# Optimization experiments

Measured on AMD Instinct MI355X. Metric: run time of the kernel, lower is better.

Reference implementation:

```python
import jax, jax.numpy as jnp
import numpy as np

T, K_FR, K_D, A = 2000, 400, 400, 100
EPS = 1e-24


def setup_inputs() -> dict:
    key = jax.random.key(0)
    ks = jax.random.split(key, 5)
    t = jnp.arange(T, dtype=jnp.float32)                      # uniform grid, dt = 1
    mask_spikes_fr = jax.random.randint(ks[0], (T, K_FR), 0, 2, dtype=jnp.int32)
    X_fr = jax.random.normal(ks[1], (T, K_FR, A), dtype=jnp.float32)
    theta = jax.random.normal(ks[2], (A,), dtype=jnp.float32) * 0.01  # keep r = exp(u) ~ O(1)
    phi_d = jax.random.normal(ks[3], (K_D,), dtype=jnp.float32)
    phi_fr = jax.random.normal(ks[4], (K_FR,), dtype=jnp.float32)
    return {"t": t, "mask_spikes_fr": mask_spikes_fr, "X_fr": X_fr,
            "theta": theta, "phi_d": phi_d, "phi_fr": phi_fr}


def _forward(t, mask_spikes_fr, X_fr, theta, phi_d, phi_fr, lam_mmd=1.0):
    dt = t[1] - t[0]
    m = mask_spikes_fr.astype(X_fr.dtype)                     # [T, K_fr] spike indicator
    u = jnp.einsum('tka,a->tk', X_fr, theta)                  # membrane potential
    r = jnp.exp(u)                                            # non_linearity = 'exp'
    # per-trial point-process log-likelihood: [K_fr]
    ll = jnp.sum(jnp.log(1.0 - jnp.exp(-dt * r) + EPS) * m - dt * r * (1.0 - m), axis=0)
    # score-function gradient of log-likelihood w.r.t. theta (r detached): [K_fr, A]
    r_d = jax.lax.stop_gradient(r)
    exp_r = jnp.exp(r_d * dt)
    g_ll = dt * jnp.einsum('tka,tk->ka', X_fr, r_d / (exp_r - 1.0 - EPS) * m) \
         - dt * jnp.einsum('tka,tk->ka', X_fr, r_d * (1.0 - m))
    # gramians from per-trial features phi
    g_ff = phi_fr[:, None] * phi_fr[None, :]                  # [K_fr, K_fr], symmetric
    g_df = phi_d[:, None] * phi_fr[None, :]                   # [K_d, K_fr]
    g_dd = phi_d[:, None] * phi_d[None, :]                    # [K_d, K_d], symmetric
    K_fr = phi_fr.shape[0]
    K_d = phi_d.shape[0]
    n_fr = K_fr * (K_fr - 1) // 2                             # number of triu (k=1) pairs
    n_d = K_d * (K_d - 1) // 2
    row_ff = jnp.sum(g_ff, axis=1)
    diag_ff = jnp.diagonal(g_ff)
    # mean over i<j of (ll_i + ll_j) * g_ff[i,j]; g_ff symmetric => (full - diag)/2
    mmd_grad = (jnp.dot(ll, row_ff) - jnp.dot(ll, diag_ff)) / n_fr \
             - 2.0 * jnp.mean(ll[None, :] * g_df)
    # mean over i<j of (g_ll_i + g_ll_j) * g_ff[i,j] per component a, minus cross term
    grad_theta = (jnp.einsum('ij,ia->a', g_ff, g_ll) - jnp.einsum('i,ia->a', diag_ff, g_ll)) / n_fr \
               - 2.0 * jnp.einsum('df,fa->a', g_df, g_ll) / (K_d * K_fr)
    # unbiased MMD: off-diagonal means of gramians
    tri_ff = (jnp.sum(g_ff) - jnp.sum(diag_ff)) / 2.0 / n_fr
    tri_dd = (jnp.sum(g_dd) - jnp.sum(jnp.diagonal(g_dd))) / 2.0 / n_d
    mmd = tri_dd + tri_ff - 2.0 * jnp.mean(g_df)
    return lam_mmd * mmd_grad, lam_mmd * grad_theta, mmd


def reference(t, mask_spikes_fr, X_fr, theta, phi_d, phi_fr):
    return _forward(t, mask_spikes_fr, X_fr, theta, phi_d, phi_fr)
```

## Files before the change

### kernel.cpp

```cpp
#include <hip/hip_runtime.h>

#define T_LEN   2000
#define K_FR    400
#define K_D     400
#define A_DIM   100
#define N_ROWS  (T_LEN * K_FR)
#define RPB     64
#define TILE_F  (RPB * A_DIM)
#define NBATCH  (N_ROWS / RPB)
#define EPSF    1e-24f
#define MAIN_BLOCKS 1024


__global__ void mmdglm_setup(const float* __restrict__ phi_d,
                             const float* __restrict__ phi_fr,
                             float* __restrict__ c,
                             float* __restrict__ gth_acc,
                             double* __restrict__ mmdg_acc,
                             float* __restrict__ out)
{
    __shared__ float w1[8], w2[8], w3[8], w4[8];
    __shared__ float sums[4];
    const int tid = threadIdx.x;
    const float vfr = (tid < K_FR) ? phi_fr[tid] : 0.f;
    const float vd  = (tid < K_D)  ? phi_d[tid]  : 0.f;
    float s1 = vfr, s2 = vfr * vfr, s3 = vd, s4 = vd * vd;
    #pragma unroll
    for (int off = 1; off < 64; off <<= 1) {
        s1 += __shfl_xor(s1, off);
        s2 += __shfl_xor(s2, off);
        s3 += __shfl_xor(s3, off);
        s4 += __shfl_xor(s4, off);
    }
    const int wave = tid >> 6, lane = tid & 63;
    if (lane == 0) { w1[wave] = s1; w2[wave] = s2; w3[wave] = s3; w4[wave] = s4; }
    __syncthreads();
    if (tid == 0) {
        float a = 0, b = 0, cc = 0, d = 0;
        for (int i = 0; i < 8; ++i) { a += w1[i]; b += w2[i]; cc += w3[i]; d += w4[i]; }
        sums[0] = a; sums[1] = b; sums[2] = cc; sums[3] = d;
    }
    __syncthreads();
    const float S_fr = sums[0], Q_fr = sums[1], S_d = sums[2], Q_d = sums[3];
    const float n_fr = (float)(K_FR * (K_FR - 1) / 2);
    const float n_d  = (float)(K_D * (K_D - 1) / 2);
    if (tid < K_FR) {
        const float p = phi_fr[tid];
        c[tid] = (S_fr * p - p * p) / n_fr
               - 2.0f * S_d * p / (float)(K_D * K_FR);
    }
    if (tid < A_DIM) gth_acc[tid] = 0.f;
    if (tid == 511) *mmdg_acc = 0.0;
    if (tid == 0) {
        const float mmd = (S_d * S_d - Q_d) / (2.0f * n_d)
                        + (S_fr * S_fr - Q_fr) / (2.0f * n_fr)
                        - 2.0f * S_d * S_fr / (float)(K_D * K_FR);
        out[101] = mmd;
    }
}

__device__ __forceinline__ void stage_tile(const float* __restrict__ g0,
                                           float* l0, int wave, int lane)
{
    for (int c = wave; c < 25; c += 4) {
        const float* g = g0 + (c << 8) + (lane << 2);
        float* l = l0 + (c << 8);
        __builtin_amdgcn_global_load_lds(
            (const __attribute__((address_space(1))) void*)g,
            (__attribute__((address_space(3))) void*)l, 16, 0, 0);
    }
}

__global__ __launch_bounds__(256)
void mmdglm_main(const float* __restrict__ X,
                 const int*   __restrict__ mask,
                 const float* __restrict__ theta,
                 const float* __restrict__ tvec,
                 const float* __restrict__ c,
                 float*  __restrict__ gth_acc,
                 double* __restrict__ mmdg_acc)
{
    __shared__ __align__(16) float buf[2][TILE_F];
    __shared__ float lred[4];
    const int tid  = threadIdx.x;
    const int wave = tid >> 6, lane = tid & 63;
    const int slot = tid >> 2;
    const int part = tid & 3;

    float th[25];
    #pragma unroll
    for (int j = 0; j < 25; ++j) th[j] = theta[part * 25 + j];

    const float dt = tvec[1] - tvec[0];

    float acc[25];
    #pragma unroll
    for (int j = 0; j < 25; ++j) acc[j] = 0.f;
    float llacc = 0.f;

    int t = blockIdx.x;
    stage_tile(X + (size_t)t * TILE_F, buf[0], wave, lane);
    int cur = 0;

    for (; t < NBATCH; t += gridDim.x) {
        __syncthreads();

        const int tn = t + (int)gridDim.x;
        if (tn < NBATCH)
            stage_tile(X + (size_t)tn * TILE_F, buf[cur ^ 1], wave, lane);

        const int row = t * RPB + slot;
        const float* xp = buf[cur] + 25 * tid;
        float x[25];
        float u = 0.f;
        #pragma unroll
        for (int j = 0; j < 25; ++j) { x[j] = xp[j]; u = fmaf(x[j], th[j], u); }
        u += __shfl_xor(u, 1);
        u += __shfl_xor(u, 2);

        const float r  = __expf(u);
        const int   m  = mask[row];
        const float ck = c[row - (row / K_FR) * K_FR];
        float w, llt;
        if (m) {
            const float eneg = __expf(-dt * r);
            const float epos = __expf(dt * r);
            llt = __logf(1.0f - eneg + EPSF);
            w   = dt * r / (epos - 1.0f - EPSF);
        } else {
            llt = -dt * r;
            w   = -dt * r;
        }
        const float cw = ck * w;
        if (part == 0) llacc = fmaf(ck, llt, llacc);
        #pragma unroll
        for (int j = 0; j < 25; ++j) acc[j] = fmaf(cw, x[j], acc[j]);

        cur ^= 1;
    }
    __syncthreads();

    float* red = &buf[0][0];
    #pragma unroll
    for (int j = 0; j < 25; ++j) red[tid * 25 + j] = acc[j];
    __syncthreads();
    if (tid < A_DIM) {
        const int p = tid / 25, j = tid - p * 25;
        float s = 0.f;
        for (int sl = 0; sl < RPB; ++sl)
            s += red[(sl * 4 + p) * 25 + j];
        atomicAdd(&gth_acc[tid], s);
    }

    float l = llacc;
    #pragma unroll
    for (int off = 1; off < 64; off <<= 1) l += __shfl_xor(l, off);
    if (lane == 0) lred[wave] = l;
    __syncthreads();
    if (tid == 0)
        atomicAdd(mmdg_acc, (double)(lred[0] + lred[1] + lred[2] + lred[3]));
}

__global__ void mmdglm_finalize(const double* __restrict__ mmdg_acc,
                                const float* __restrict__ gth_acc,
                                float* __restrict__ out)
{
    const int tid = threadIdx.x;
    if (tid == 0) out[0] = (float)(*mmdg_acc);
    if (tid >= 1 && tid <= 100) out[tid] = gth_acc[tid - 1];
}

extern "C" void kernel_launch(void* const* d_in, const int* in_sizes, int n_in,
                              void* d_out, int out_size, void* d_ws, size_t ws_size,
                              hipStream_t stream) {
    const float* t      = (const float*)d_in[0];
    const int*   mask   = (const int*)  d_in[1];
    const float* X      = (const float*)d_in[2];
    const float* theta  = (const float*)d_in[3];
    const float* phi_d  = (const float*)d_in[4];
    const float* phi_fr = (const float*)d_in[5];
    float* out = (float*)d_out;

    char* ws = (char*)d_ws;
    double* mmdg_acc = (double*)ws;
    float*  gth_acc  = (float*)(ws + 8);
    float*  c        = (float*)(ws + 416);

    mmdglm_setup<<<1, 512, 0, stream>>>(phi_d, phi_fr, c, gth_acc, mmdg_acc, out);
    mmdglm_main<<<MAIN_BLOCKS, 256, 0, stream>>>(X, mask, theta, t, c, gth_acc, mmdg_acc);
    mmdglm_finalize<<<1, 128, 0, stream>>>(mmdg_acc, gth_acc, out);
}
```

Measured before the change: 458.2 us.

## Fold setup into main kernel and replace atomics with per-block partials

Removes the separate setup kernel: every block now recomputes the phi sums itself and derives the per-trial coefficient inline, while its first tile load is already in flight. Global atomics are replaced by per-block partial sums written to workspace and reduced by a wider multi-block finalize kernel. The grid drops to 768 blocks with a launch-bounds occupancy hint of 3 blocks per CU. This saves one kernel launch and the atomic contention, at the cost of redundant phi reductions in every block.

```diff
diff --git a/kernel.cpp b/kernel.cpp
--- a/kernel.cpp
+++ b/kernel.cpp
@@ -9,55 +9,8 @@
 #define TILE_F  (RPB * A_DIM)
 #define NBATCH  (N_ROWS / RPB)
 #define EPSF    1e-24f
-#define MAIN_BLOCKS 1024
+#define GRID    768
 
-
-__global__ void mmdglm_setup(const float* __restrict__ phi_d,
-                             const float* __restrict__ phi_fr,
-                             float* __restrict__ c,
-                             float* __restrict__ gth_acc,
-                             double* __restrict__ mmdg_acc,
-                             float* __restrict__ out)
-{
-    __shared__ float w1[8], w2[8], w3[8], w4[8];
-    __shared__ float sums[4];
-    const int tid = threadIdx.x;
-    const float vfr = (tid < K_FR) ? phi_fr[tid] : 0.f;
-    const float vd  = (tid < K_D)  ? phi_d[tid]  : 0.f;
-    float s1 = vfr, s2 = vfr * vfr, s3 = vd, s4 = vd * vd;
-    #pragma unroll
-    for (int off = 1; off < 64; off <<= 1) {
-        s1 += __shfl_xor(s1, off);
-        s2 += __shfl_xor(s2, off);
-        s3 += __shfl_xor(s3, off);
-        s4 += __shfl_xor(s4, off);
-    }
-    const int wave = tid >> 6, lane = tid & 63;
-    if (lane == 0) { w1[wave] = s1; w2[wave] = s2; w3[wave] = s3; w4[wave] = s4; }
-    __syncthreads();
-    if (tid == 0) {
-        float a = 0, b = 0, cc = 0, d = 0;
-        for (int i = 0; i < 8; ++i) { a += w1[i]; b += w2[i]; cc += w3[i]; d += w4[i]; }
-        sums[0] = a; sums[1] = b; sums[2] = cc; sums[3] = d;
-    }
-    __syncthreads();
-    const float S_fr = sums[0], Q_fr = sums[1], S_d = sums[2], Q_d = sums[3];
-    const float n_fr = (float)(K_FR * (K_FR - 1) / 2);
-    const float n_d  = (float)(K_D * (K_D - 1) / 2);
-    if (tid < K_FR) {
-        const float p = phi_fr[tid];
-        c[tid] = (S_fr * p - p * p) / n_fr
-               - 2.0f * S_d * p / (float)(K_D * K_FR);
-    }
-    if (tid < A_DIM) gth_acc[tid] = 0.f;
-    if (tid == 511) *mmdg_acc = 0.0;
-    if (tid == 0) {
-        const float mmd = (S_d * S_d - Q_d) / (2.0f * n_d)
-                        + (S_fr * S_fr - Q_fr) / (2.0f * n_fr)
-                        - 2.0f * S_d * S_fr / (float)(K_D * K_FR);
-        out[101] = mmd;
-    }
-}
 
 __device__ __forceinline__ void stage_tile(const float* __restrict__ g0,
                                            float* l0, int wave, int lane)
@@ -71,21 +24,55 @@
     }
 }
 
-__global__ __launch_bounds__(256)
+__global__ __launch_bounds__(256, 3)
 void mmdglm_main(const float* __restrict__ X,
                  const int*   __restrict__ mask,
                  const float* __restrict__ theta,
                  const float* __restrict__ tvec,
-                 const float* __restrict__ c,
-                 float*  __restrict__ gth_acc,
-                 double* __restrict__ mmdg_acc)
+                 const float* __restrict__ phi_d,
+                 const float* __restrict__ phi_fr,
+                 float* __restrict__ ws_g,
+                 float* __restrict__ ws_ll,
+                 float* __restrict__ out)
 {
     __shared__ __align__(16) float buf[2][TILE_F];
-    __shared__ float lred[4];
+    __shared__ float psum[4][4];
+    __shared__ float lsum[4];
     const int tid  = threadIdx.x;
     const int wave = tid >> 6, lane = tid & 63;
     const int slot = tid >> 2;
     const int part = tid & 3;
+    const int bid  = blockIdx.x;
+
+    stage_tile(X + (size_t)bid * TILE_F, buf[0], wave, lane);
+
+    float s1 = 0.f, s2 = 0.f, s3 = 0.f, s4 = 0.f;
+    for (int i = tid; i < K_FR; i += 256) { const float p = phi_fr[i]; s1 += p; s2 += p * p; }
+    for (int i = tid; i < K_D;  i += 256) { const float p = phi_d[i];  s3 += p; s4 += p * p; }
+    #pragma unroll
+    for (int off = 1; off < 64; off <<= 1) {
+        s1 += __shfl_xor(s1, off);
+        s2 += __shfl_xor(s2, off);
+        s3 += __shfl_xor(s3, off);
+        s4 += __shfl_xor(s4, off);
+    }
+    if (lane == 0) { psum[0][wave] = s1; psum[1][wave] = s2; psum[2][wave] = s3; psum[3][wave] = s4; }
+    __syncthreads();
+    const float S_fr = psum[0][0] + psum[0][1] + psum[0][2] + psum[0][3];
+    const float S_d  = psum[2][0] + psum[2][1] + psum[2][2] + psum[2][3];
+
+    const float n_fr    = (float)(K_FR * (K_FR - 1) / 2);
+    const float inv_nfr = 1.0f / n_fr;
+    const float C2      = S_d * (2.0f / (float)(K_D * K_FR));
+
+    if (bid == 0 && tid == 0) {
+        const float Q_fr = psum[1][0] + psum[1][1] + psum[1][2] + psum[1][3];
+        const float Q_d  = psum[3][0] + psum[3][1] + psum[3][2] + psum[3][3];
+        const float n_d  = (float)(K_D * (K_D - 1) / 2);
+        out[101] = (S_d * S_d - Q_d) / (2.0f * n_d)
+                 + (S_fr * S_fr - Q_fr) / (2.0f * n_fr)
+                 - 2.0f * S_d * S_fr / (float)(K_D * K_FR);
+    }
 
     float th[25];
     #pragma unroll
@@ -98,14 +85,11 @@
     for (int j = 0; j < 25; ++j) acc[j] = 0.f;
     float llacc = 0.f;
 
-    int t = blockIdx.x;
-    stage_tile(X + (size_t)t * TILE_F, buf[0], wave, lane);
     int cur = 0;
-
-    for (; t < NBATCH; t += gridDim.x) {
+    for (int t = bid; t < NBATCH; t += GRID) {
         __syncthreads();
 
-        const int tn = t + (int)gridDim.x;
+        const int tn = t + GRID;
         if (tn < NBATCH)
             stage_tile(X + (size_t)tn * TILE_F, buf[cur ^ 1], wave, lane);
 
@@ -120,7 +104,9 @@
 
         const float r  = __expf(u);
         const int   m  = mask[row];
-        const float ck = c[row - (row / K_FR) * K_FR];
+        const int   rk = row - (row / K_FR) * K_FR;
+        const float p  = phi_fr[rk];
+        const float ck = p * ((S_fr - p) * inv_nfr - C2);
         float w, llt;
         if (m) {
             const float eneg = __expf(-dt * r);
@@ -145,29 +131,47 @@
     for (int j = 0; j < 25; ++j) red[tid * 25 + j] = acc[j];
     __syncthreads();
     if (tid < A_DIM) {
-        const int p = tid / 25, j = tid - p * 25;
+        const int pq = tid / 25, j = tid - pq * 25;
         float s = 0.f;
         for (int sl = 0; sl < RPB; ++sl)
-            s += red[(sl * 4 + p) * 25 + j];
-        atomicAdd(&gth_acc[tid], s);
+            s += red[(sl * 4 + pq) * 25 + j];
+        ws_g[tid * GRID + bid] = s;
     }
 
     float l = llacc;
     #pragma unroll
     for (int off = 1; off < 64; off <<= 1) l += __shfl_xor(l, off);
-    if (lane == 0) lred[wave] = l;
+    if (lane == 0) lsum[wave] = l;
     __syncthreads();
     if (tid == 0)
-        atomicAdd(mmdg_acc, (double)(lred[0] + lred[1] + lred[2] + lred[3]));
+        ws_ll[bid] = lsum[0] + lsum[1] + lsum[2] + lsum[3];
 }
 
-__global__ void mmdglm_finalize(const double* __restrict__ mmdg_acc,
-                                const float* __restrict__ gth_acc,
-                                float* __restrict__ out)
+__global__ __launch_bounds__(256)
+void mmdglm_finalize(const float* __restrict__ ws_g,
+                     const float* __restrict__ ws_ll,
+                     float* __restrict__ out)
 {
-    const int tid = threadIdx.x;
-    if (tid == 0) out[0] = (float)(*mmdg_acc);
-    if (tid >= 1 && tid <= 100) out[tid] = gth_acc[tid - 1];
+    __shared__ float fr[4];
+    __shared__ double dr[4];
+    const int tid = threadIdx.x, wave = tid >> 6, lane = tid & 63;
+    const int b = blockIdx.x;
+    if (b < A_DIM) {
+        const float* p = ws_g + (size_t)b * GRID;
+        float s = p[tid] + p[tid + 256] + p[tid + 512];
+        #pragma unroll
+        for (int off = 1; off < 64; off <<= 1) s += __shfl_xor(s, off);
+        if (lane == 0) fr[wave] = s;
+        __syncthreads();
+        if (tid == 0) out[1 + b] = fr[0] + fr[1] + fr[2] + fr[3];
+    } else {
+        double d = (double)ws_ll[tid] + (double)ws_ll[tid + 256] + (double)ws_ll[tid + 512];
+        #pragma unroll
+        for (int off = 1; off < 64; off <<= 1) d += __shfl_xor(d, off);
+        if (lane == 0) dr[wave] = d;
+        __syncthreads();
+        if (tid == 0) out[0] = (float)(dr[0] + dr[1] + dr[2] + dr[3]);
+    }
 }
 
 extern "C" void kernel_launch(void* const* d_in, const int* in_sizes, int n_in,
@@ -181,12 +185,10 @@
     const float* phi_fr = (const float*)d_in[5];
     float* out = (float*)d_out;
 
-    char* ws = (char*)d_ws;
-    double* mmdg_acc = (double*)ws;
-    float*  gth_acc  = (float*)(ws + 8);
-    float*  c        = (float*)(ws + 416);
+    float* ws_g  = (float*)d_ws;
+    float* ws_ll = (float*)((char*)d_ws + (size_t)A_DIM * GRID * sizeof(float));
 
-    mmdglm_setup<<<1, 512, 0, stream>>>(phi_d, phi_fr, c, gth_acc, mmdg_acc, out);
-    mmdglm_main<<<MAIN_BLOCKS, 256, 0, stream>>>(X, mask, theta, t, c, gth_acc, mmdg_acc);
-    mmdglm_finalize<<<1, 128, 0, stream>>>(mmdg_acc, gth_acc, out);
+    mmdglm_main<<<GRID, 256, 0, stream>>>(X, mask, theta, t, phi_d, phi_fr,
+                                          ws_g, ws_ll, out);
+    mmdglm_finalize<<<A_DIM + 1, 256, 0, stream>>>(ws_g, ws_ll, out);
 }
```

Result: faster. 436.2 us (-4.8%).
